# Performance work log

Measured on AMD Instinct MI355X. Metric: run time of the kernel, lower is better.

## Reference

```python
import jax, jax.numpy as jnp
import numpy as np


def setup_inputs() -> dict:
    key = jax.random.key(0)
    k1, k2, k3, k4, k5 = jax.random.split(key, 5)
    V, E = 512, 256  # num_nodes, num_edges
    l_v = jax.random.normal(k1, (V,), dtype=jnp.float32)
    h = jax.random.randint(k2, (E, V), 0, 2, dtype=jnp.int32)  # binary parity-check matrix
    s_c = jax.random.randint(k3, (E,), 0, 2).astype(jnp.float32)  # syndrome bits in {0,1}
    b = jax.random.uniform(k4, (V,), dtype=jnp.float32)
    w = jax.random.uniform(k5, (V, E), dtype=jnp.float32)
    return {"l_v": l_v, "h": h, "s_c": s_c, "b": b, "w": w, "iterations": 5}


def reference(l_v, h, s_c, b, w, iterations):
    V = l_v.shape[0]
    E = s_c.shape[0]
    hT = h.T                                   # [V, E] entries (used as indices, values in {0,1})
    v_idx = jnp.arange(V)[:, None]             # [V, 1]
    c_idx = jnp.arange(E)[:, None]             # [E, 1]
    sign_c = (1.0 - 2.0 * s_c)[:, None]        # (-1)**s_c for s in {0,1}
    base = (l_v * b)[:, None]                  # [V, 1]

    mu_vc = jnp.zeros((V, E), dtype=jnp.float32)  # v -> c messages
    mu_cv = jnp.zeros((E, V), dtype=jnp.float32)  # c -> v messages

    for _ in range(int(iterations)):
        # ---- v -> c: message[v,c] = tanh(0.5*(l_v[v]*b[v] + sum_{e: h[e,v]!=c} mu_cv[h[e,v],v]*w[v,h[e,v]]))
        contrib = mu_cv[hT, v_idx] * w[v_idx, hT]          # [V, E]: term for each row e of h
        total = contrib.sum(axis=1, keepdims=True)          # [V, 1]
        # subtract terms where the index value h[e,v] equals the target check c (scatter-add)
        sub = jnp.zeros((V, E), dtype=jnp.float32).at[v_idx, hT].add(contrib)  # [V, E]
        mu_vc_new = jnp.tanh(0.5 * (base + total - sub))    # [V, E]

        # ---- c -> v: message[c,v] = (-1)**s_c * 2*atanh(prod_{j: h[c,j]!=v} tanh(mu_vc[h[c,j],c]/2))
        tvals = jnp.tanh(0.5 * mu_vc[h, c_idx])             # [E, V] per-entry tanh terms
        # mask out entries whose value equals target v, then product over j
        masked = jnp.where(h[:, None, :] == jnp.arange(V)[None, :, None],
                           jnp.float32(1.0), tvals[:, None, :])  # [E, V, V]
        prod = masked.prod(axis=2)                          # [E, V]
        mu_cv_new = sign_c * 2.0 * jnp.arctanh(prod)        # [E, V]

        mu_vc, mu_cv = mu_vc_new, mu_cv_new

    # ---- marginalization (no exclusion)
    contrib = mu_cv[hT, v_idx] * w[v_idx, hT]               # [V, E]
    mu_v = jnp.tanh(0.5 * (l_v * b + contrib.sum(axis=1)))  # [V]
    return 1.0 / (jnp.exp(mu_v) + 1.0)
```

## Files before the change

### kernel.cpp

```cpp
#include <hip/hip_runtime.h>
#include <math.h>


#define V_N 512
#define E_N 256
#define BLK1 32

__device__ inline float tanh_f(float x) {
    float xx = fminf(fmaxf(2.0f * x, -80.0f), 80.0f);
    float e = __expf(xx);
    return __fdividef(e - 1.0f, e + 1.0f);
}
__device__ inline float atanh_f(float x) {
    return 0.5f * __logf(__fdividef(1.0f + x, 1.0f - x));
}
__device__ inline float powi_f(float t, int n) {
    if (n <= 0) return 1.0f;
    float p = __powf(fabsf(t), (float)n);
    if ((n & 1) && t < 0.0f) p = -p;
    return p;
}

__global__ __launch_bounds__(256) void bp_count(const int* __restrict__ h,
                                                int* __restrict__ ws) {
    const int b = blockIdx.x, t = threadIdx.x;
    const int cg = t & 127;
    const int rh = t >> 7;
    const int4* h4 = (const int4*)h;
    const int rowbase = b * 8 + rh * 4;
    int4 acc = make_int4(0, 0, 0, 0);
    #pragma unroll
    for (int r = 0; r < 4; ++r) {
        int4 x = h4[(rowbase + r) * (V_N / 4) + cg];
        acc.x += x.x; acc.y += x.y; acc.z += x.z; acc.w += x.w;
    }
    __shared__ int4 p[2][128];
    p[rh][cg] = acc;
    __syncthreads();
    if (t < 128) {
        int4 a = p[0][t], c = p[1][t];
        ((int4*)ws)[b * 128 + t] =
            make_int4(a.x + c.x, a.y + c.y, a.z + c.z, a.w + c.w);
    }
}

__global__ __launch_bounds__(512) void bp_solve(
    const float* __restrict__ l_v, const int* __restrict__ h,
    const float* __restrict__ s_c, const float* __restrict__ b,
    const float* __restrict__ w, const int* __restrict__ it_p,
    const int* __restrict__ ws, float* __restrict__ out)
{
    const int v = threadIdx.x;

    __shared__ int cntsh[V_N];
    __shared__ int wred[8][2];
    __shared__ float csh[8];

    int cnt = 0;
    #pragma unroll
    for (int bb = 0; bb < BLK1; ++bb)
        cnt += ws[bb * V_N + v];
    cntsh[v] = cnt;

    int r0 = h[v], r1 = h[V_N + v];
    #pragma unroll
    for (int off = 32; off > 0; off >>= 1) {
        r0 += __shfl_down(r0, off);
        r1 += __shfl_down(r1, off);
    }
    if ((v & 63) == 0) { wred[v >> 6][0] = r0; wred[v >> 6][1] = r1; }
    __syncthreads();

    if (v == 0) {
        int n1_0 = 0, n1_1 = 0;
        #pragma unroll
        for (int wv = 0; wv < 8; ++wv) { n1_0 += wred[wv][0]; n1_1 += wred[wv][1]; }
        const int iters = it_p[0];
        const int n0_0 = V_N - n1_0, n0_1 = V_N - n1_1;
        const int cnt1_0 = cntsh[0], cnt1_1 = cntsh[1];
        const int cnt0_0 = E_N - cnt1_0, cnt0_1 = E_N - cnt1_1;
        const float base0 = l_v[0] * b[0];
        const float base1 = l_v[1] * b[1];
        const float w00 = w[0],     w01 = w[1];
        const float w10 = w[E_N],   w11 = w[E_N + 1];
        const float sg0 = 1.0f - 2.0f * s_c[0];
        const float sg1 = 1.0f - 2.0f * s_c[1];

        float V0c0 = 0.f, V0c1 = 0.f, V1c0 = 0.f, V1c1 = 0.f;
        float C0v0 = 0.f, C0v1 = 0.f, C0vR = 0.f;
        float C1v0 = 0.f, C1v1 = 0.f, C1vR = 0.f;

        for (int it = 0; it < iters; ++it) {
            float T0 = (float)cnt0_0 * C0v0 * w00;
            float T1 = (float)cnt1_0 * C1v0 * w01;
            float nV0c0 = tanh_f(0.5f * (base0 + T1));
            float nV0c1 = tanh_f(0.5f * (base0 + T0));
            T0 = (float)cnt0_1 * C0v1 * w10;
            T1 = (float)cnt1_1 * C1v1 * w11;
            float nV1c0 = tanh_f(0.5f * (base1 + T1));
            float nV1c1 = tanh_f(0.5f * (base1 + T0));

            float t0 = tanh_f(0.5f * V0c0);
            float t1 = tanh_f(0.5f * V1c0);
            float p0 = powi_f(t0, n0_0);
            float p1 = powi_f(t1, n1_0);
            float nC0v0 = sg0 * 2.0f * atanh_f(p1);
            float nC0v1 = sg0 * 2.0f * atanh_f(p0);
            float nC0vR = sg0 * 2.0f * atanh_f(p0 * p1);
            t0 = tanh_f(0.5f * V0c1);
            t1 = tanh_f(0.5f * V1c1);
            p0 = powi_f(t0, n0_1);
            p1 = powi_f(t1, n1_1);
            float nC1v0 = sg1 * 2.0f * atanh_f(p1);
            float nC1v1 = sg1 * 2.0f * atanh_f(p0);
            float nC1vR = sg1 * 2.0f * atanh_f(p0 * p1);

            V0c0 = nV0c0; V0c1 = nV0c1; V1c0 = nV1c0; V1c1 = nV1c1;
            C0v0 = nC0v0; C0v1 = nC0v1; C0vR = nC0vR;
            C1v0 = nC1v0; C1v1 = nC1v1; C1vR = nC1vR;
        }
        csh[0] = C0v0; csh[1] = C0v1; csh[2] = C0vR;
        csh[3] = C1v0; csh[4] = C1v1; csh[5] = C1vR;
    }
    __syncthreads();

    {
        const int cnt1 = cntsh[v];
        const int cnt0 = E_N - cnt1;
        const float basev = l_v[v] * b[v];
        const float wv0 = w[v * E_N + 0];
        const float wv1 = w[v * E_N + 1];
        const float c0 = (v == 0) ? csh[0] : (v == 1) ? csh[1] : csh[2];
        const float c1 = (v == 0) ? csh[3] : (v == 1) ? csh[4] : csh[5];
        const float s = basev + (float)cnt0 * c0 * wv0 + (float)cnt1 * c1 * wv1;
        const float mu = tanh_f(0.5f * s);
        out[v] = __fdividef(1.0f, __expf(mu) + 1.0f);
    }
}

extern "C" void kernel_launch(void* const* d_in, const int* in_sizes, int n_in,
                              void* d_out, int out_size, void* d_ws, size_t ws_size,
                              hipStream_t stream) {
    const float* l_v   = (const float*)d_in[0];
    const int*   h     = (const int*)  d_in[1];
    const float* s_c   = (const float*)d_in[2];
    const float* b     = (const float*)d_in[3];
    const float* w     = (const float*)d_in[4];
    const int*   iters = (const int*)  d_in[5];
    float* out = (float*)d_out;
    int*   ws  = (int*)d_ws;

    hipLaunchKernelGGL(bp_count, dim3(BLK1), dim3(256), 0, stream, h, ws);
    hipLaunchKernelGGL(bp_solve, dim3(1), dim3(512), 0, stream,
                       l_v, h, s_c, b, w, iters, ws, out);
}
```

Baseline: 23.03 us.

## Fuse count and solve kernels using global flag handoff to block zero

Result: no change. 22.73 us (-1.3%).

```diff
diff --git a/kernel.cpp b/kernel.cpp
--- a/kernel.cpp
+++ b/kernel.cpp
@@ -4,7 +4,7 @@
 
 #define V_N 512
 #define E_N 256
-#define BLK1 32
+#define NBLK 32
 
 __device__ inline float tanh_f(float x) {
     float xx = fminf(fmaxf(2.0f * x, -80.0f), 80.0f);
@@ -21,66 +21,79 @@
     return p;
 }
 
-__global__ __launch_bounds__(256) void bp_count(const int* __restrict__ h,
-                                                int* __restrict__ ws) {
-    const int b = blockIdx.x, t = threadIdx.x;
-    const int cg = t & 127;
-    const int rh = t >> 7;
-    const int4* h4 = (const int4*)h;
-    const int rowbase = b * 8 + rh * 4;
-    int4 acc = make_int4(0, 0, 0, 0);
-    #pragma unroll
-    for (int r = 0; r < 4; ++r) {
-        int4 x = h4[(rowbase + r) * (V_N / 4) + cg];
-        acc.x += x.x; acc.y += x.y; acc.z += x.z; acc.w += x.w;
+__global__ __launch_bounds__(256) void bp_fused(
+    const float* __restrict__ l_v, const int* __restrict__ h,
+    const float* __restrict__ s_c, const float* __restrict__ b_,
+    const float* __restrict__ w, const int* __restrict__ it_p,
+    int* ws, float* __restrict__ out)
+{
+    const int blk = blockIdx.x, t = threadIdx.x;
+    int* flags = ws + NBLK * V_N;
+
+    {
+        const int cg = t & 127;
+        const int rh = t >> 7;
+        const int4* h4 = (const int4*)h;
+        const int rowbase = blk * 8 + rh * 4;
+        int4 acc = make_int4(0, 0, 0, 0);
+        #pragma unroll
+        for (int r = 0; r < 4; ++r) {
+            int4 x = h4[(rowbase + r) * (V_N / 4) + cg];
+            acc.x += x.x; acc.y += x.y; acc.z += x.z; acc.w += x.w;
+        }
+        __shared__ int4 p[2][128];
+        p[rh][cg] = acc;
+        __syncthreads();
+        if (t < 128) {
+            int4 a = p[0][t], c = p[1][t];
+            ((int4*)ws)[blk * 128 + t] =
+                make_int4(a.x + c.x, a.y + c.y, a.z + c.z, a.w + c.w);
+        }
     }
-    __shared__ int4 p[2][128];
-    p[rh][cg] = acc;
+    __threadfence();
     __syncthreads();
-    if (t < 128) {
-        int4 a = p[0][t], c = p[1][t];
-        ((int4*)ws)[b * 128 + t] =
-            make_int4(a.x + c.x, a.y + c.y, a.z + c.z, a.w + c.w);
+    if (t == 0) atomicExch(&flags[blk], 1);
+    if (blk != 0) return;
+
+    if (t < NBLK) {
+        while (atomicAdd(&flags[t], 0) != 1) { }
     }
-}
-
-__global__ __launch_bounds__(512) void bp_solve(
-    const float* __restrict__ l_v, const int* __restrict__ h,
-    const float* __restrict__ s_c, const float* __restrict__ b,
-    const float* __restrict__ w, const int* __restrict__ it_p,
-    const int* __restrict__ ws, float* __restrict__ out)
-{
-    const int v = threadIdx.x;
+    __syncthreads();
+    __threadfence();
 
     __shared__ int cntsh[V_N];
-    __shared__ int wred[8][2];
+    __shared__ int wred[4][2];
     __shared__ float csh[8];
 
-    int cnt = 0;
+    int c0s = 0, c1s = 0;
     #pragma unroll
-    for (int bb = 0; bb < BLK1; ++bb)
-        cnt += ws[bb * V_N + v];
-    cntsh[v] = cnt;
+    for (int bb = 0; bb < NBLK; ++bb) {
+        c0s += ws[bb * V_N + t];
+        c1s += ws[bb * V_N + t + 256];
+    }
+    cntsh[t] = c0s;
+    cntsh[t + 256] = c1s;
 
-    int r0 = h[v], r1 = h[V_N + v];
+    int r0 = h[t] + h[t + 256];
+    int r1 = h[V_N + t] + h[V_N + t + 256];
     #pragma unroll
     for (int off = 32; off > 0; off >>= 1) {
         r0 += __shfl_down(r0, off);
         r1 += __shfl_down(r1, off);
     }
-    if ((v & 63) == 0) { wred[v >> 6][0] = r0; wred[v >> 6][1] = r1; }
+    if ((t & 63) == 0) { wred[t >> 6][0] = r0; wred[t >> 6][1] = r1; }
     __syncthreads();
 
-    if (v == 0) {
+    if (t == 0) {
         int n1_0 = 0, n1_1 = 0;
         #pragma unroll
-        for (int wv = 0; wv < 8; ++wv) { n1_0 += wred[wv][0]; n1_1 += wred[wv][1]; }
+        for (int wv = 0; wv < 4; ++wv) { n1_0 += wred[wv][0]; n1_1 += wred[wv][1]; }
         const int iters = it_p[0];
         const int n0_0 = V_N - n1_0, n0_1 = V_N - n1_1;
         const int cnt1_0 = cntsh[0], cnt1_1 = cntsh[1];
         const int cnt0_0 = E_N - cnt1_0, cnt0_1 = E_N - cnt1_1;
-        const float base0 = l_v[0] * b[0];
-        const float base1 = l_v[1] * b[1];
+        const float base0 = l_v[0] * b_[0];
+        const float base1 = l_v[1] * b_[1];
         const float w00 = w[0],     w01 = w[1];
         const float w10 = w[E_N],   w11 = w[E_N + 1];
         const float sg0 = 1.0f - 2.0f * s_c[0];
@@ -124,10 +137,12 @@
     }
     __syncthreads();
 
-    {
+    #pragma unroll
+    for (int k = 0; k < 2; ++k) {
+        const int v = t + k * 256;
         const int cnt1 = cntsh[v];
         const int cnt0 = E_N - cnt1;
-        const float basev = l_v[v] * b[v];
+        const float basev = l_v[v] * b_[v];
         const float wv0 = w[v * E_N + 0];
         const float wv1 = w[v * E_N + 1];
         const float c0 = (v == 0) ? csh[0] : (v == 1) ? csh[1] : csh[2];
@@ -136,6 +151,8 @@
         const float mu = tanh_f(0.5f * s);
         out[v] = __fdividef(1.0f, __expf(mu) + 1.0f);
     }
+
+    if (t < NBLK) atomicExch(&flags[t], 0);
 }
 
 extern "C" void kernel_launch(void* const* d_in, const int* in_sizes, int n_in,
@@ -150,7 +167,6 @@
     float* out = (float*)d_out;
     int*   ws  = (int*)d_ws;
 
-    hipLaunchKernelGGL(bp_count, dim3(BLK1), dim3(256), 0, stream, h, ws);
-    hipLaunchKernelGGL(bp_solve, dim3(1), dim3(512), 0, stream,
+    hipLaunchKernelGGL(bp_fused, dim3(NBLK), dim3(256), 0, stream,
                        l_v, h, s_c, b, w, iters, ws, out);
 }
```
